# Kernel tuning notes

Measured on AMD Instinct MI355X. Metric: run time of the kernel, lower is better.

Reference implementation:

```python
import jax, jax.numpy as jnp
import numpy as np

B, C, H, W = 8, 512, 64, 64
K = 8
NUM = K * K          # number of channel groups / graph nodes
CG = C // NUM        # channels per group (8)
NC = 19              # num_classes
OUT = 512            # bottleneck out_channels


def make_dct_weight():
    # Per-channel 2D DCT basis. Channel ch belongs to group g = ch // CG;
    # group g selects frequency (u, v) = (g % K, g // K).
    g = np.arange(C) // CG
    u = (g % K).astype(np.float64)
    v = (g // K).astype(np.float64)
    th = (np.arange(H) + 0.5) / H   # [H]
    tw = (np.arange(W) + 0.5) / W   # [W]
    bh = np.cos(np.pi * u[:, None] * th[None, :])  # [C,H]
    bw = np.cos(np.pi * v[:, None] * tw[None, :])  # [C,W]
    return (bh[:, :, None] * bw[:, None, :]).astype(np.float32)  # [C,H,W]


def setup_inputs() -> dict:
    key = jax.random.key(0)
    ks = jax.random.split(key, 10)
    s = lambda i, shape: jax.random.normal(ks[i], shape, jnp.float32) * 0.05
    return {
        'x': jax.random.normal(ks[0], (B, C, H, W), jnp.float32),
        'dct_w': jnp.asarray(make_dct_weight()),
        'dm_w1': s(1, (CG, CG)),
        'dm_gamma': jnp.ones((CG,), jnp.float32),
        'dm_beta': jnp.zeros((CG,), jnp.float32),
        'dm_w2': s(2, (NC, CG)),
        'dm_b2': s(3, (NC,)),
        'fuse_w': s(4, (NUM,)),
        'fuse_b': s(5, (1,)),
        'gcn_w1': s(6, (NUM, NUM)),
        'gcn_w2': s(7, (CG, CG)),
        'bot_w': s(8, (OUT, 2 * C, 3, 3)),
        'bot_gamma': jnp.ones((OUT,), jnp.float32),
        'bot_beta': jnp.zeros((OUT,), jnp.float32),
    }


def reference(x, dct_w, dm_w1, dm_gamma, dm_beta, dm_w2, dm_b2,
              fuse_w, fuse_b, gcn_w1, gcn_w2, bot_w, bot_gamma, bot_beta):
    # MultiSpectralDCTLayer: elementwise DCT basis multiply, keeps [B,C,H,W]
    fres = x * dct_w[None]

    # channel_split -> grouped layout [B, NUM, CG, H*W]
    xg = x.reshape(B, NUM, CG, H * W)
    fg = fres.reshape(B, NUM, CG, H * W)

    # decoder_map: 1x1 conv -> BN(eval, mean=0,var=1) -> ReLU -> (Dropout=id) -> 1x1 conv
    h1 = jnp.einsum('dc,bncp->bndp', dm_w1, fg)
    h1 = jax.nn.relu(h1 * dm_gamma[None, None, :, None] + dm_beta[None, None, :, None])
    fres_map = jnp.einsum('kc,bncp->bnkp', dm_w2, h1) + dm_b2[None, None, :, None]  # [B,n,NC,HW]

    # fuse: 1x1 conv over group dim n -> [B,NC,H,W]
    fres_map_output = (jnp.einsum('n,bnkp->bkp', fuse_w, fres_map) + fuse_b[0]).reshape(B, NC, H, W)

    # local frequency class centers: [B,n,NC,HW] @ [B,n,HW,c] -> [B,n,NC,c]
    fHWc = fg.transpose(0, 1, 3, 2)   # [B,n,HW,c]
    xHWc = xg.transpose(0, 1, 3, 2)   # [B,n,HW,c]
    local = jnp.einsum('bnkp,bnpc->bnkc', fres_map, fHWc)

    # GCN over n (node) dim: conv1 + residual ReLU, then Linear over c
    g = jnp.einsum('mn,bnkc->bmkc', gcn_w1, local)
    g = jax.nn.relu(g + local)
    local = jnp.einsum('bnkc,dc->bnkd', g, gcn_w2)

    # attention combine: softmax(x @ local^T) @ local
    wm = jax.nn.softmax(jnp.einsum('bnpc,bnkc->bnpk', xHWc, local), axis=-1)  # [B,n,HW,NC]
    out = jnp.einsum('bnpk,bnkc->bnpc', wm, local)  # [B,n,HW,c]

    # channel_recover -> [B,C,H,W]
    out = out.transpose(0, 1, 3, 2).reshape(B, C, H, W)

    # bottleneck: 3x3 conv on concat, BN(eval) affine, ReLU
    cat = jnp.concatenate([x, out], axis=1)  # [B,2C,H,W]
    y = jax.lax.conv_general_dilated(cat, bot_w, (1, 1), 'SAME',
                                     dimension_numbers=('NCHW', 'OIHW', 'NCHW'))
    y = jax.nn.relu(y * bot_gamma[None, :, None, None] + bot_beta[None, :, None, None])
    return (y, fres_map_output)
```

## Files before the change

kernel.cpp:

```cpp
#include <hip/hip_runtime.h>


typedef __attribute__((ext_vector_type(8))) unsigned short u16x8;
typedef __attribute__((ext_vector_type(8))) __bf16 bf16x8;
typedef __attribute__((ext_vector_type(4))) float f32x4;

__device__ inline unsigned short f2bf(float f) {
    unsigned int u = __float_as_uint(f);
    u += 0x7fffu + ((u >> 16) & 1u);
    return (unsigned short)(u >> 16);
}

__device__ __forceinline__ void gload16(unsigned short* lds, const unsigned short* g) {
    __builtin_amdgcn_global_load_lds(
        (const __attribute__((address_space(1))) unsigned int*)g,
        (__attribute__((address_space(3))) unsigned int*)lds, 16, 0, 0);
}

__global__ __launch_bounds__(256) void repack_w(const float* __restrict__ w,
                                                unsigned short* __restrict__ wt) {
    __shared__ float buf[9216];
    const int oc = blockIdx.x;
    const int tid = threadIdx.x;
    const float* src = w + (size_t)oc * 9216;
    for (int i = tid; i < 9216; i += 256) buf[i] = src[i];
    __syncthreads();
#pragma unroll
    for (int t = 0; t < 9; ++t) {
        for (int i = tid; i < 1024; i += 256)
            wt[((size_t)t * 512 + oc) * 1024 + i] = f2bf(buf[i * 9 + t]);
    }
}

__global__ __launch_bounds__(256) void front_kernel(
    const float* __restrict__ x, const float* __restrict__ dct,
    const float* __restrict__ w1, const float* __restrict__ gamma,
    const float* __restrict__ beta, const float* __restrict__ w2,
    const float* __restrict__ b2, const float* __restrict__ fuse_w,
    float* __restrict__ part, float* __restrict__ fpart,
    unsigned short* __restrict__ cat) {
    __shared__ __align__(16) float fgs[8][260];
    __shared__ __align__(16) float fms[19][260];
    __shared__ float sw1[64], sw2[152], sb2[19], sg[8], sb[8], sfw[64];
    const int bid = blockIdx.x;
    const int sp = bid >> 7;
    const int b = (bid >> 4) & 7;
    const int ch = bid & 15;
    const int tid = threadIdx.x;
    if (tid < 64) { sw1[tid] = w1[tid]; sfw[tid] = fuse_w[tid]; }
    if (tid < 152) sw2[tid] = w2[tid];
    if (tid < 19) sb2[tid] = b2[tid];
    if (tid < 8) { sg[tid] = gamma[tid]; sb[tid] = beta[tid]; }
    __syncthreads();
    const int p = ch * 256 + tid;
    const int kk = tid >> 3, cc = tid & 7;
    float facc[19];
#pragma unroll
    for (int k = 0; k < 19; ++k) facc[k] = 0.f;
    for (int nn = 0; nn < 16; ++nn) {
        const int n = sp * 16 + nn;
        float fg[8];
        u16x8 xw;
#pragma unroll
        for (int c = 0; c < 8; ++c) {
            const float xv = x[((size_t)(b * 512 + n * 8 + c)) * 4096 + p];
            fg[c] = xv * dct[((size_t)(n * 8 + c)) * 4096 + p];
            xw[c] = f2bf(xv);
            fgs[c][tid] = fg[c];
        }
        *(u16x8*)(cat + ((size_t)(b * 4096) + p) * 1024 + n * 8) = xw;
        float h1[8];
#pragma unroll
        for (int d = 0; d < 8; ++d) {
            float s = 0.f;
#pragma unroll
            for (int c = 0; c < 8; ++c) s = fmaf(sw1[d * 8 + c], fg[c], s);
            h1[d] = fmaxf(fmaf(s, sg[d], sb[d]), 0.f);
        }
        const float fw = sfw[n];
#pragma unroll
        for (int k = 0; k < 19; ++k) {
            float s = sb2[k];
#pragma unroll
            for (int d = 0; d < 8; ++d) s = fmaf(sw2[k * 8 + d], h1[d], s);
            fms[k][tid] = s;
            facc[k] = fmaf(fw, s, facc[k]);
        }
        __syncthreads();
        if (tid < 152) {
            float accv = 0.f;
#pragma unroll 8
            for (int p4 = 0; p4 < 256; p4 += 4) {
                const float4 a = *(const float4*)&fms[kk][p4];
                const float4 g4 = *(const float4*)&fgs[cc][p4];
                accv += a.x * g4.x + a.y * g4.y + a.z * g4.z + a.w * g4.w;
            }
            part[((size_t)((b * 64 + n) * 16) + ch) * 152 + tid] = accv;
        }
        __syncthreads();
    }
#pragma unroll
    for (int k = 0; k < 19; ++k)
        fpart[((size_t)(sp * 8 + b) * 19 + k) * 4096 + p] = facc[k];
}

__global__ __launch_bounds__(256) void fuse_reduce(
    const float* __restrict__ fpart, const float* __restrict__ fuse_b,
    float* __restrict__ out1) {
    const int i = blockIdx.x * 256 + threadIdx.x;
    float s = fuse_b[0];
#pragma unroll
    for (int sp = 0; sp < 4; ++sp) s += fpart[(size_t)sp * 622592 + i];
    out1[i] = s;
}

__global__ __launch_bounds__(256) void gcn_kernel(
    const float* __restrict__ part, const float* __restrict__ w1,
    const float* __restrict__ w2, float* __restrict__ local2) {
    __shared__ float L[9728];
    __shared__ float R[9728];
    __shared__ float sw1[4096];
    __shared__ float sw2[64];
    const int b = blockIdx.x;
    const int tid = threadIdx.x;
    for (int i = tid; i < 4096; i += 256) sw1[i] = w1[i];
    if (tid < 64) sw2[tid] = w2[tid];
    for (int i = tid; i < 9728; i += 256) {
        int n = i / 152, t = i - n * 152;
        float s = 0.f;
#pragma unroll
        for (int ch = 0; ch < 16; ++ch)
            s += part[((size_t)((b * 64 + n) * 16) + ch) * 152 + t];
        L[i] = s;
    }
    __syncthreads();
    for (int i = tid; i < 9728; i += 256) {
        int m = i / 152, t = i - m * 152;
        float g = 0.f;
        for (int n = 0; n < 64; ++n) g = fmaf(sw1[m * 64 + n], L[n * 152 + t], g);
        R[i] = fmaxf(g + L[i], 0.f);
    }
    __syncthreads();
    for (int i = tid; i < 9728; i += 256) {
        int n = i / 152, t = i - n * 152;
        int k = t >> 3, d = t & 7;
        float s = 0.f;
#pragma unroll
        for (int c = 0; c < 8; ++c) s = fmaf(R[n * 152 + k * 8 + c], sw2[d * 8 + c], s);
        local2[(size_t)b * 9728 + i] = s;
    }
}

__global__ __launch_bounds__(256) void attn_kernel(
    const float* __restrict__ x, const float* __restrict__ local2,
    unsigned short* __restrict__ cat) {
    __shared__ float L[152];
    const int bn = blockIdx.x;
    const int b = bn >> 6, n = bn & 63;
    const int tid = threadIdx.x;
    if (tid < 152) L[tid] = local2[(size_t)bn * 152 + tid];
    __syncthreads();
    for (int i = 0; i < 16; ++i) {
        const int p = i * 256 + tid;
        float xv[8];
#pragma unroll
        for (int c = 0; c < 8; ++c)
            xv[c] = x[((size_t)(b * 512 + n * 8 + c)) * 4096 + p];
        float lg[19];
        float mx = -1e30f;
#pragma unroll
        for (int k = 0; k < 19; ++k) {
            float s = 0.f;
#pragma unroll
            for (int c = 0; c < 8; ++c) s = fmaf(xv[c], L[k * 8 + c], s);
            lg[k] = s;
            mx = fmaxf(mx, s);
        }
        float se = 0.f;
#pragma unroll
        for (int k = 0; k < 19; ++k) {
            lg[k] = __expf(lg[k] - mx);
            se += lg[k];
        }
        const float inv = 1.f / se;
        float ov[8];
#pragma unroll
        for (int c = 0; c < 8; ++c) ov[c] = 0.f;
#pragma unroll
        for (int k = 0; k < 19; ++k) {
#pragma unroll
            for (int c = 0; c < 8; ++c) ov[c] = fmaf(lg[k], L[k * 8 + c], ov[c]);
        }
        u16x8 w;
#pragma unroll
        for (int c = 0; c < 8; ++c) w[c] = f2bf(ov[c] * inv);
        *(u16x8*)(cat + ((size_t)(b * 4096) + p) * 1024 + 512 + n * 8) = w;
    }
}

__global__ __launch_bounds__(512, 1) void conv_kernel(
    const unsigned short* __restrict__ cat, const unsigned short* __restrict__ wt,
    const unsigned short* __restrict__ zp,
    const float* __restrict__ gamma, const float* __restrict__ beta,
    float* __restrict__ out) {
    __shared__ __align__(16) unsigned short As[2 * 16384];
    __shared__ __align__(16) unsigned short Bs[2 * 16384];
    const int bid0 = blockIdx.x;
    const int bid = (bid0 & 7) * 32 + (bid0 >> 3);
    const int mt = bid >> 1;
    const int nt = bid & 1;
    const int b = mt >> 4;
    const int pix0 = (mt & 15) * 256;
    const int y0 = (mt & 15) * 4;
    const int ocb = nt * 256;
    const int tid = threadIdx.x;
    const int w = tid >> 6;
    const int lane = tid & 63;
    const int l16 = lane & 15;
    const int khalf = lane >> 4;
    const int wrow = (w >> 2) * 64;
    const int wcol = (w & 3) * 32;
    const int sx = tid >> 3;
    const int icsw = ((tid & 7) ^ ((tid >> 3) & 7)) * 8;
    const unsigned short* zps = zp + icsw;
    const unsigned short* catb = cat + ((size_t)b * 4096) * 1024 + icsw;
    int colks[2];
#pragma unroll
    for (int ks = 0; ks < 2; ++ks)
        colks[ks] = ((ks * 64 + khalf * 16) ^ ((l16 & 7) << 4)) >> 1;

    f32x4 acc[2][2][4][2];
#pragma unroll
    for (int qm = 0; qm < 2; ++qm)
#pragma unroll
        for (int qn = 0; qn < 2; ++qn)
#pragma unroll
            for (int m = 0; m < 4; ++m)
#pragma unroll
                for (int n = 0; n < 2; ++n)
#pragma unroll
                    for (int j = 0; j < 4; ++j) acc[qm][qn][m][n][j] = 0.f;

    bf16x8 af[4][2];
    bf16x8 bq[2][2];

#define STAGE_A(SP, SH, DY, XOK, AB)                                               \
    _Pragma("unroll") for (int j_ = 0; j_ < 2; ++j_) {                             \
        const int yy_ = y0 + (SH) * 2 + j_ + (DY);                                 \
        const unsigned short* src_ =                                               \
            ((XOK) && ((unsigned)yy_ < 64u)) ? (AB) + yy_ * 65536 : zps;           \
        gload16(As + (SP) * 16384 + (SH) * 8192 + (j_ * 512 + tid) * 8, src_);     \
    }

#define STAGE_B(SP, SH, WB)                                                        \
    _Pragma("unroll") for (int j_ = 0; j_ < 2; ++j_) {                             \
        gload16(Bs + (SP) * 16384 + (SH) * 8192 + (j_ * 512 + tid) * 8,            \
                (WB) + (SH) * 131072 + j_ * 65536);                                \
    }

#define READ_AF(PE, QM)                                                            \
    _Pragma("unroll") for (int m_ = 0; m_ < 4; ++m_)                               \
        _Pragma("unroll") for (int ks_ = 0; ks_ < 2; ++ks_)                        \
            af[m_][ks_] = *(const bf16x8*)(As + (PE) * 16384 +                     \
                ((QM) * 128 + wrow + m_ * 16 + l16) * 64 + colks[ks_]);

#define READ_BF(PE, QN)                                                            \
    _Pragma("unroll") for (int n_ = 0; n_ < 2; ++n_)                               \
        _Pragma("unroll") for (int ks_ = 0; ks_ < 2; ++ks_)                        \
            bq[n_][ks_] = *(const bf16x8*)(Bs + (PE) * 16384 +                     \
                ((QN) * 128 + wcol + n_ * 16 + l16) * 64 + colks[ks_]);

#define SYNC_PHASE(VN)                                                             \
    asm volatile("s_waitcnt vmcnt(" #VN ")" ::: "memory");                         \
    __builtin_amdgcn_s_barrier();                                                  \
    __builtin_amdgcn_sched_barrier(0);

#define MFMA_Q(QM, QN)                                                             \
    __builtin_amdgcn_s_setprio(1);                                                 \
    _Pragma("unroll") for (int m_ = 0; m_ < 4; ++m_)                               \
        _Pragma("unroll") for (int n_ = 0; n_ < 2; ++n_)                           \
            _Pragma("unroll") for (int ks_ = 0; ks_ < 2; ++ks_)                    \
                acc[QM][QN][m_][n_] = __builtin_amdgcn_mfma_f32_16x16x32_bf16(     \
                    af[m_][ks_], bq[n_][ks_], acc[QM][QN][m_][n_], 0, 0, 0);       \
    __builtin_amdgcn_s_setprio(0);

    {
        const bool xok_p = sx >= 1;
        const unsigned short* ab_p = catb + (sx - 1) * 1024;
        const unsigned short* wb_p = wt + (size_t)(ocb + sx) * 1024 + icsw;
        STAGE_A(0, 0, -1, xok_p, ab_p);
        STAGE_B(0, 0, wb_p);
        STAGE_B(0, 1, wb_p);
        STAGE_A(0, 1, -1, xok_p, ab_p);
    }
    SYNC_PHASE(4)

    for (int i = 0; i < 72; ++i) {
        const int kto = 2 * i + 1;
        const int ktn = (i == 71) ? 0 : 2 * i + 2;
        const int tap_o = kto >> 4;
        const int dy_o = tap_o / 3 - 1;
        const int dx_o = tap_o % 3 - 1;
        const int ic_o = (kto & 15) << 6;
        const bool xok_o = (unsigned)(sx + dx_o) < 64u;
        const unsigned short* ab_o = catb + (sx + dx_o) * 1024 + ic_o;
        const unsigned short* wb_o = wt + ((size_t)tap_o << 19) +
                                     (size_t)(ocb + sx) * 1024 + ic_o + icsw;
        const int tap_n = ktn >> 4;
        const int dy_n = tap_n / 3 - 1;
        const int dx_n = tap_n % 3 - 1;
        const int ic_n = (ktn & 15) << 6;
        const bool xok_n = (unsigned)(sx + dx_n) < 64u;
        const unsigned short* ab_n = catb + (sx + dx_n) * 1024 + ic_n;
        const unsigned short* wb_n = wt + ((size_t)tap_n << 19) +
                                     (size_t)(ocb + sx) * 1024 + ic_n + icsw;
        READ_AF(0, 0) READ_BF(0, 0)
        STAGE_A(1, 0, dy_o, xok_o, ab_o);
        SYNC_PHASE(4)
        MFMA_Q(0, 0)
        READ_BF(0, 1)
        STAGE_B(1, 0, wb_o);
        SYNC_PHASE(4)
        MFMA_Q(0, 1)
        READ_AF(0, 1) READ_BF(0, 0)
        STAGE_B(1, 1, wb_o);
        SYNC_PHASE(6)
        MFMA_Q(1, 0)
        READ_BF(0, 1)
        STAGE_A(1, 1, dy_o, xok_o, ab_o);
        SYNC_PHASE(4)
        MFMA_Q(1, 1)
        READ_AF(1, 0) READ_BF(1, 0)
        STAGE_A(0, 0, dy_n, xok_n, ab_n);
        SYNC_PHASE(4)
        MFMA_Q(0, 0)
        READ_BF(1, 1)
        STAGE_B(0, 0, wb_n);
        SYNC_PHASE(4)
        MFMA_Q(0, 1)
        READ_AF(1, 1) READ_BF(1, 0)
        STAGE_B(0, 1, wb_n);
        SYNC_PHASE(6)
        MFMA_Q(1, 0)
        READ_BF(1, 1)
        STAGE_A(0, 1, dy_n, xok_n, ab_n);
        SYNC_PHASE(4)
        MFMA_Q(1, 1)
    }
    asm volatile("s_waitcnt vmcnt(0)" ::: "memory");

#pragma unroll
    for (int qn = 0; qn < 2; ++qn)
#pragma unroll
        for (int n = 0; n < 2; ++n) {
            const int oc = ocb + qn * 128 + wcol + n * 16 + l16;
            const float g = gamma[oc], bb = beta[oc];
#pragma unroll
            for (int qm = 0; qm < 2; ++qm)
#pragma unroll
                for (int m = 0; m < 4; ++m) {
                    const int P = qm * 128 + wrow + m * 16 + khalf * 4;
                    float4 o;
                    o.x = fmaxf(fmaf(acc[qm][qn][m][n][0], g, bb), 0.f);
                    o.y = fmaxf(fmaf(acc[qm][qn][m][n][1], g, bb), 0.f);
                    o.z = fmaxf(fmaf(acc[qm][qn][m][n][2], g, bb), 0.f);
                    o.w = fmaxf(fmaf(acc[qm][qn][m][n][3], g, bb), 0.f);
                    *(float4*)(out + ((size_t)(b * 512 + oc)) * 4096 + pix0 + P) = o;
                }
        }
#undef STAGE_A
#undef STAGE_B
#undef READ_AF
#undef READ_BF
#undef SYNC_PHASE
#undef MFMA_Q
}

extern "C" void kernel_launch(void* const* d_in, const int* in_sizes, int n_in,
                              void* d_out, int out_size, void* d_ws, size_t ws_size,
                              hipStream_t stream) {
    const float* x = (const float*)d_in[0];
    const float* dct = (const float*)d_in[1];
    const float* dm_w1 = (const float*)d_in[2];
    const float* dm_g = (const float*)d_in[3];
    const float* dm_b = (const float*)d_in[4];
    const float* dm_w2 = (const float*)d_in[5];
    const float* dm_b2 = (const float*)d_in[6];
    const float* fuse_w = (const float*)d_in[7];
    const float* fuse_b = (const float*)d_in[8];
    const float* gcn_w1 = (const float*)d_in[9];
    const float* gcn_w2 = (const float*)d_in[10];
    const float* bot_w = (const float*)d_in[11];
    const float* bot_g = (const float*)d_in[12];
    const float* bot_b = (const float*)d_in[13];

    float* y = (float*)d_out;
    float* out1 = y + (size_t)8 * 512 * 4096;
    float* part = y;
    float* fpart = y + 1245184;

    char* ws = (char*)d_ws;
    const size_t CAT_BYTES = (size_t)8 * 4096 * 1024 * 2;
    const size_t WT_BYTES = (size_t)9 * 512 * 1024 * 2;
    const size_t PART_BYTES = (size_t)2048 * 152 * 4;
    const size_t L2_BYTES = (size_t)8 * 9728 * 4;
    const size_t ZP_BYTES = 4096;
    if (ws_size < CAT_BYTES + WT_BYTES + PART_BYTES + L2_BYTES + ZP_BYTES) return;

    unsigned short* cat = (unsigned short*)ws;
    unsigned short* wt = (unsigned short*)(ws + CAT_BYTES);
    float* local2 = (float*)(ws + CAT_BYTES + WT_BYTES + PART_BYTES);
    unsigned short* zp = (unsigned short*)(ws + CAT_BYTES + WT_BYTES + PART_BYTES + L2_BYTES);

    hipMemsetAsync(zp, 0, ZP_BYTES, stream);
    front_kernel<<<dim3(512), dim3(256), 0, stream>>>(x, dct, dm_w1, dm_g, dm_b,
                                                      dm_w2, dm_b2, fuse_w,
                                                      part, fpart, cat);
    fuse_reduce<<<dim3(2432), dim3(256), 0, stream>>>(fpart, fuse_b, out1);
    gcn_kernel<<<dim3(8), dim3(256), 0, stream>>>(part, gcn_w1, gcn_w2, local2);
    repack_w<<<dim3(512), dim3(256), 0, stream>>>(bot_w, wt);
    attn_kernel<<<dim3(512), dim3(256), 0, stream>>>(x, local2, cat);
    conv_kernel<<<dim3(256), dim3(512), 0, stream>>>(cat, wt, zp, bot_g, bot_b, y);
}
```

Before: 454.0 us.

## Reuse input halo rows across 3x3 taps in conv, staging only weights per tap

Restructures the implicit-GEMM conv loop so each 64-channel slice loads a 6-row input halo into LDS once. All nine taps then read shifted windows from it, with x-offsets clamped and edge lanes zeroed, instead of re-staging the A tile for every tap. Only the weight tile is double-buffered per tap, and the next channel slice's rows are prefetched into alternate row slots. This is meant to cut global and LDS fill traffic for the activation operand by about 9x. In exchange it adds per-lane address clamping and zeroing logic, a more intricate vmcnt schedule, and some risk of LDS bank conflicts on the shifted reads.

```diff
diff --git a/kernel.cpp b/kernel.cpp
--- a/kernel.cpp
+++ b/kernel.cpp
@@ -203,7 +203,7 @@
     const unsigned short* __restrict__ zp,
     const float* __restrict__ gamma, const float* __restrict__ beta,
     float* __restrict__ out) {
-    __shared__ __align__(16) unsigned short As[2 * 16384];
+    __shared__ __align__(16) unsigned short As[10 * 4096];
     __shared__ __align__(16) unsigned short Bs[2 * 16384];
     const int bid0 = blockIdx.x;
     const int bid = (bid0 & 7) * 32 + (bid0 >> 3);
@@ -218,16 +218,19 @@
     const int lane = tid & 63;
     const int l16 = lane & 15;
     const int khalf = lane >> 4;
-    const int wrow = (w >> 2) * 64;
+    const int wr1 = w >> 2;
+    const int wrow = wr1 * 64;
     const int wcol = (w & 3) * 32;
     const int sx = tid >> 3;
     const int icsw = ((tid & 7) ^ ((tid >> 3) & 7)) * 8;
     const unsigned short* zps = zp + icsw;
     const unsigned short* catb = cat + ((size_t)b * 4096) * 1024 + icsw;
-    int colks[2];
-#pragma unroll
-    for (int ks = 0; ks < 2; ++ks)
-        colks[ks] = ((ks * 64 + khalf * 16) ^ ((l16 & 7) << 4)) >> 1;
+    int colk[3][2];
+#pragma unroll
+    for (int d = 0; d < 3; ++d)
+#pragma unroll
+        for (int ks = 0; ks < 2; ++ks)
+            colk[d][ks] = ((ks * 64 + khalf * 16) ^ (((l16 + d - 1) & 7) << 4)) >> 1;
 
     f32x4 acc[2][2][4][2];
 #pragma unroll
@@ -243,39 +246,47 @@
 
     bf16x8 af[4][2];
     bf16x8 bq[2][2];
-
-#define STAGE_A(SP, SH, DY, XOK, AB)                                               \
-    _Pragma("unroll") for (int j_ = 0; j_ < 2; ++j_) {                             \
-        const int yy_ = y0 + (SH) * 2 + j_ + (DY);                                 \
-        const unsigned short* src_ =                                               \
-            ((XOK) && ((unsigned)yy_ < 64u)) ? (AB) + yy_ * 65536 : zps;           \
-        gload16(As + (SP) * 16384 + (SH) * 8192 + (j_ * 512 + tid) * 8, src_);     \
-    }
-
-#define STAGE_B(SP, SH, WB)                                                        \
-    _Pragma("unroll") for (int j_ = 0; j_ < 2; ++j_) {                             \
-        gload16(Bs + (SP) * 16384 + (SH) * 8192 + (j_ * 512 + tid) * 8,            \
-                (WB) + (SH) * 131072 + j_ * 65536);                                \
-    }
-
-#define READ_AF(PE, QM)                                                            \
-    _Pragma("unroll") for (int m_ = 0; m_ < 4; ++m_)                               \
-        _Pragma("unroll") for (int ks_ = 0; ks_ < 2; ++ks_)                        \
-            af[m_][ks_] = *(const bf16x8*)(As + (PE) * 16384 +                     \
-                ((QM) * 128 + wrow + m_ * 16 + l16) * 64 + colks[ks_]);
-
-#define READ_BF(PE, QN)                                                            \
+    const bf16x8 zf = {};
+
+#define AF_READ(QM, DY, DX)                                                        \
+    {                                                                              \
+        const int r_ = (QM) * 2 + wr1 + (DY) + 1;                                  \
+        const int phys_ = (r_ < 2) ? r_ : r_ + 4 * cp;                             \
+        const int rb_ = phys_ * 4096;                                              \
+        _Pragma("unroll") for (int m_ = 0; m_ < 4; ++m_) {                         \
+            const int xm_ = m_ * 16 + l16 + (DX);                                  \
+            const int xc_ = ((DX) == 0) ? xm_ : min(max(xm_, 0), 63);              \
+            const int ab_ = rb_ + xc_ * 64;                                        \
+            _Pragma("unroll") for (int ks_ = 0; ks_ < 2; ++ks_)                    \
+                af[m_][ks_] = *(const bf16x8*)(As + ab_ + colk[(DX) + 1][ks_]);    \
+            if ((DX) == -1 && m_ == 0 && l16 == 0) { af[0][0] = zf; af[0][1] = zf; } \
+            if ((DX) == 1 && m_ == 3 && l16 == 15) { af[3][0] = zf; af[3][1] = zf; } \
+        }                                                                          \
+    }
+
+#define BQ_READ(SOFF, QN)                                                          \
     _Pragma("unroll") for (int n_ = 0; n_ < 2; ++n_)                               \
         _Pragma("unroll") for (int ks_ = 0; ks_ < 2; ++ks_)                        \
-            bq[n_][ks_] = *(const bf16x8*)(Bs + (PE) * 16384 +                     \
-                ((QN) * 128 + wcol + n_ * 16 + l16) * 64 + colks[ks_]);
-
-#define SYNC_PHASE(VN)                                                             \
-    asm volatile("s_waitcnt vmcnt(" #VN ")" ::: "memory");                         \
-    __builtin_amdgcn_s_barrier();                                                  \
-    __builtin_amdgcn_sched_barrier(0);
-
-#define MFMA_Q(QM, QN)                                                             \
+            bq[n_][ks_] = *(const bf16x8*)(Bs + (SOFF) +                           \
+                ((QN) * 128 + wcol + n_ * 16 + l16) * 64 + colk[1][ks_]);
+
+#define STAGE_BH(H, SWOFF, TAP, ICB)                                               \
+    _Pragma("unroll") for (int j_ = 0; j_ < 2; ++j_) {                             \
+        gload16(Bs + (SWOFF) + (H) * 8192 + (j_ * 512 + tid) * 8,                  \
+                wt + (size_t)(TAP) * 524288 +                                      \
+                    (size_t)(ocb + (H) * 128 + j_ * 64 + sx) * 1024 + (ICB) + icsw); \
+    }
+
+#define STAGE_AROW(R)                                                              \
+    do {                                                                           \
+        const int yy_ = y0 - 1 + (R);                                              \
+        const int ph_ = ((R) < 2) ? (R) : (R) + 4 * cp1;                           \
+        const unsigned short* s2_ = ((unsigned)yy_ < 64u)                          \
+            ? catb + ((size_t)(yy_ * 64 + sx)) * 1024 + iccn : zps;                \
+        gload16(As + ph_ * 4096 + tid * 8, s2_);                                   \
+    } while (0)
+
+#define MFMA16(QM, QN)                                                             \
     __builtin_amdgcn_s_setprio(1);                                                 \
     _Pragma("unroll") for (int m_ = 0; m_ < 4; ++m_)                               \
         _Pragma("unroll") for (int n_ = 0; n_ < 2; ++n_)                           \
@@ -284,68 +295,61 @@
                     af[m_][ks_], bq[n_][ks_], acc[QM][QN][m_][n_], 0, 0, 0);       \
     __builtin_amdgcn_s_setprio(0);
 
+#define VWAIT(N)                                                                   \
+    asm volatile("s_waitcnt vmcnt(" #N ")" ::: "memory");                          \
+    __builtin_amdgcn_sched_barrier(0);
+
+#define TAP_BODY(T, DY, DX, AROW, W0N, W2N)                                        \
+    {                                                                              \
+        const int s_ = (c + (T)) & 1;                                              \
+        const int sr_ = s_ << 14;                                                  \
+        const int sw_ = sr_ ^ 16384;                                               \
+        const int tn_ = ((T) == 8) ? 0 : (T) + 1;                                  \
+        const int icb_ = ((T) == 8) ? iccn : icc;                                  \
+                                                                 \
+        VWAIT(W0N)                                                                 \
+        __builtin_amdgcn_s_barrier();                                              \
+        __builtin_amdgcn_sched_barrier(0);                                         \
+        AF_READ(0, DY, DX)                                                         \
+        BQ_READ(sr_, 0)                                                            \
+        STAGE_BH(0, sw_, tn_, icb_)                                                \
+        MFMA16(0, 0)                                                               \
+                                                                 \
+        AF_READ(1, DY, DX)                                                         \
+        if ((AROW) >= 0) STAGE_AROW(AROW);                                         \
+        MFMA16(1, 0)                                                               \
+                                                                 \
+        VWAIT(W2N)                                                                 \
+        BQ_READ(sr_, 1)                                                            \
+        STAGE_BH(1, sw_, tn_, icb_)                                                \
+        MFMA16(1, 1)                                                               \
+                                                                 \
+        AF_READ(0, DY, DX)                                                         \
+        MFMA16(0, 1)                                                               \
+    }
+
     {
-        const bool xok_p = sx >= 1;
-        const unsigned short* ab_p = catb + (sx - 1) * 1024;
-        const unsigned short* wb_p = wt + (size_t)(ocb + sx) * 1024 + icsw;
-        STAGE_A(0, 0, -1, xok_p, ab_p);
-        STAGE_B(0, 0, wb_p);
-        STAGE_B(0, 1, wb_p);
-        STAGE_A(0, 1, -1, xok_p, ab_p);
-    }
-    SYNC_PHASE(4)
-
-    for (int i = 0; i < 72; ++i) {
-        const int kto = 2 * i + 1;
-        const int ktn = (i == 71) ? 0 : 2 * i + 2;
-        const int tap_o = kto >> 4;
-        const int dy_o = tap_o / 3 - 1;
-        const int dx_o = tap_o % 3 - 1;
-        const int ic_o = (kto & 15) << 6;
-        const bool xok_o = (unsigned)(sx + dx_o) < 64u;
-        const unsigned short* ab_o = catb + (sx + dx_o) * 1024 + ic_o;
-        const unsigned short* wb_o = wt + ((size_t)tap_o << 19) +
-                                     (size_t)(ocb + sx) * 1024 + ic_o + icsw;
-        const int tap_n = ktn >> 4;
-        const int dy_n = tap_n / 3 - 1;
-        const int dx_n = tap_n % 3 - 1;
-        const int ic_n = (ktn & 15) << 6;
-        const bool xok_n = (unsigned)(sx + dx_n) < 64u;
-        const unsigned short* ab_n = catb + (sx + dx_n) * 1024 + ic_n;
-        const unsigned short* wb_n = wt + ((size_t)tap_n << 19) +
-                                     (size_t)(ocb + sx) * 1024 + ic_n + icsw;
-        READ_AF(0, 0) READ_BF(0, 0)
-        STAGE_A(1, 0, dy_o, xok_o, ab_o);
-        SYNC_PHASE(4)
-        MFMA_Q(0, 0)
-        READ_BF(0, 1)
-        STAGE_B(1, 0, wb_o);
-        SYNC_PHASE(4)
-        MFMA_Q(0, 1)
-        READ_AF(0, 1) READ_BF(0, 0)
-        STAGE_B(1, 1, wb_o);
-        SYNC_PHASE(6)
-        MFMA_Q(1, 0)
-        READ_BF(0, 1)
-        STAGE_A(1, 1, dy_o, xok_o, ab_o);
-        SYNC_PHASE(4)
-        MFMA_Q(1, 1)
-        READ_AF(1, 0) READ_BF(1, 0)
-        STAGE_A(0, 0, dy_n, xok_n, ab_n);
-        SYNC_PHASE(4)
-        MFMA_Q(0, 0)
-        READ_BF(1, 1)
-        STAGE_B(0, 0, wb_n);
-        SYNC_PHASE(4)
-        MFMA_Q(0, 1)
-        READ_AF(1, 1) READ_BF(1, 0)
-        STAGE_B(0, 1, wb_n);
-        SYNC_PHASE(6)
-        MFMA_Q(1, 0)
-        READ_BF(1, 1)
-        STAGE_A(0, 1, dy_n, xok_n, ab_n);
-        SYNC_PHASE(4)
-        MFMA_Q(1, 1)
+        const int cp1 = 0, iccn = 0;
+#pragma unroll
+        for (int r = 0; r < 6; ++r) STAGE_AROW(r);
+    }
+    STAGE_BH(0, 0, 0, 0)
+    STAGE_BH(1, 0, 0, 0)
+
+    for (int c = 0; c < 16; ++c) {
+        const int cp = c & 1;
+        const int cp1 = cp ^ 1;
+        const int icc = c << 6;
+        const int iccn = ((c + 1) & 15) << 6;
+        TAP_BODY(0, -1, -1, -1, 2, 2)
+        TAP_BODY(1, -1, 0, -1, 2, 2)
+        TAP_BODY(2, -1, 1, -1, 2, 2)
+        TAP_BODY(3, 0, -1, 0, 2, 3)
+        TAP_BODY(4, 0, 0, 2, 3, 3)
+        TAP_BODY(5, 0, 1, 3, 3, 3)
+        TAP_BODY(6, 1, -1, 1, 3, 3)
+        TAP_BODY(7, 1, 0, 4, 3, 3)
+        TAP_BODY(8, 1, 1, 5, 3, 3)
     }
     asm volatile("s_waitcnt vmcnt(0)" ::: "memory");
 
@@ -368,12 +372,13 @@
                     *(float4*)(out + ((size_t)(b * 512 + oc)) * 4096 + pix0 + P) = o;
                 }
         }
-#undef STAGE_A
-#undef STAGE_B
-#undef READ_AF
-#undef READ_BF
-#undef SYNC_PHASE
-#undef MFMA_Q
+#undef AF_READ
+#undef BQ_READ
+#undef STAGE_BH
+#undef STAGE_AROW
+#undef MFMA16
+#undef VWAIT
+#undef TAP_BODY
 }
 
 extern "C" void kernel_launch(void* const* d_in, const int* in_sizes, int n_in,
```

Result: faster. 410.1 us (-9.7%).
